# Kernel optimization log

Measured on AMD Instinct MI355X. Metric: run time of the kernel, lower is better.

The kernel has to match this reference:

```python
import jax, jax.numpy as jnp
import numpy as np

HEADS = 8


def setup_inputs() -> dict:
    key = jax.random.key(0)
    ks = jax.random.split(key, 6)
    dim = 256
    s = 0.02
    return {
        "x": jax.random.normal(ks[0], (8, dim, 32, 32), jnp.float32),
        "w_qkv": jax.random.normal(ks[1], (3 * dim, dim), jnp.float32) * s,
        "w_out": jax.random.normal(ks[2], (dim, dim), jnp.float32) * s,
        "b_out": jnp.zeros((dim,), jnp.float32),
        "w_g1": jax.random.normal(ks[3], (dim // 4, dim), jnp.float32) * s,
        "b_g1": jnp.zeros((dim // 4,), jnp.float32),
        "w_g2": jax.random.normal(ks[4], (1, dim // 4), jnp.float32) * s,
        "b_g2": jnp.zeros((1,), jnp.float32),
    }


def _conv1x1(t, w, bias=None):
    # 1x1 conv == channel matmul
    y = jnp.einsum('bchw,oc->bohw', t, w)
    if bias is not None:
        y = y + bias[None, :, None, None]
    return y


def _forward(x, w_qkv, w_out, b_out, w_g1, b_g1, w_g2, b_g2):
    b, c, h, w = x.shape
    heads = HEADS
    d = c // heads
    n = h * w
    m = min(h, w)
    scale = d ** (-0.5)

    qkv = _conv1x1(x, w_qkv)  # [b, 3c, h, w]

    def to_heads(t):  # 'b (h d) x y -> b h (x y) d'
        return t.reshape(b, heads, d, n).transpose(0, 1, 3, 2)

    q, k, v = (to_heads(t) for t in jnp.split(qkv, 3, axis=1))

    attn = jax.nn.softmax(jnp.einsum('bhid,bhjd->bhij', q, k) * scale, axis=-1)

    # diagonal branch (anti-diagonal scores are computed in the original but
    # never used in the output -> omitted as dead code)
    q2d = q.reshape(b, heads, h, w, d)
    k2d = k.reshape(b, heads, h, w, d)
    q_dm = jnp.diagonal(q2d, axis1=2, axis2=3)  # [b, heads, d, m]
    k_dm = jnp.diagonal(k2d, axis1=2, axis2=3)
    diag_main = jnp.einsum('bhnd,bhmd->bhnm', q_dm, k_dm) * scale  # [b, heads, d, d]
    diag_vec = jnp.diagonal(diag_main.mean(axis=1), axis1=-2, axis2=-1)  # [b, d]
    diag_vec = jnp.pad(diag_vec, ((0, 0), (0, n - m)))  # [b, n] (d == m)

    DIAG_WEIGHT = 0.3
    enhanced = attn + DIAG_WEIGHT * diag_vec[:, None, :, None]

    out = jnp.einsum('bhij,bhjd->bhid', enhanced, v)  # [b, heads, n, d]
    out = out.reshape(b, heads, h, w, d).transpose(0, 1, 4, 2, 3).reshape(b, c, h, w)

    # left/right asymmetry gate
    mid = w // 2
    left = x[:, :, :, :mid]
    right = x[:, :, :, mid:]
    asym = jnp.abs(left - right[:, :, :, ::-1])  # [b, c, h, w/2]
    # adaptive_avg_pool2d (h, w/2) -> (h, w) with even w == width repeat by 2
    pooled = jnp.repeat(asym, 2, axis=3)
    g = _conv1x1(pooled, w_g1, b_g1)
    g = jax.nn.gelu(g, approximate=False)
    g = jax.nn.sigmoid(_conv1x1(g, w_g2, b_g2))  # [b, 1, h, w]

    out = out * (1.0 + g)
    return _conv1x1(out, w_out, b_out)


def reference(x, w_qkv, w_out, b_out, w_g1, b_g1, w_g2, b_g2):
    return _forward(x, w_qkv, w_out, b_out, w_g1, b_g1, w_g2, b_g2)
```

## Files before the change

### kernel.cpp

```cpp
#include <hip/hip_runtime.h>
#include <hip/hip_bf16.h>
#include <math.h>

#define B 8
#define C 256
#define HEADS 8
#define D 32
#define NPIX 1024
#define OC 768
#define SCALE 0.17677669529663687f
#define LOG2E 1.4426950408889634f

typedef unsigned int uint;
typedef unsigned short u16;
typedef __attribute__((ext_vector_type(8))) short bf16x8;
typedef __attribute__((ext_vector_type(4))) short bf16x4;
typedef __attribute__((ext_vector_type(4))) float f32x4;

static __device__ inline u16 f2bf(float f) {
  uint u = __float_as_uint(f);
  return (u16)((u + 0x7fffu + ((u >> 16) & 1u)) >> 16);
}
static __device__ inline float bfval(u16 v) { return __uint_as_float((uint)v << 16); }
static __device__ inline float bf_lo(uint u) { return __uint_as_float(u << 16); }
static __device__ inline float bf_hi(uint u) { return __uint_as_float(u & 0xffff0000u); }

static __device__ inline uint pk2(float lo, float hi) {
  union { __hip_bfloat162 h; uint u; } cv;
  cv.h = __float22bfloat162_rn(float2{lo, hi});
  return cv.u;
}

__global__ __launch_bounds__(256) void k_prep(
    const float* __restrict__ x, const float* __restrict__ wqkv,
    const float* __restrict__ wout,
    u16* __restrict__ WQ, u16* __restrict__ WO, u16* __restrict__ XT) {
  const int bid = blockIdx.x, t = threadIdx.x;
  __shared__ u16 tile[64][65];
  if (bid < 256) {
    const float* src;
    u16* dst;
    int base;
    if (bid < 192) { src = wqkv; dst = WQ; base = bid * 1024; }
    else           { src = wout; dst = WO; base = (bid - 192) * 1024; }
    float4 v = *(const float4*)(src + base + t * 4);
    uint2 pk = make_uint2((uint)f2bf(v.x) | ((uint)f2bf(v.y) << 16),
                          (uint)f2bf(v.z) | ((uint)f2bf(v.w) << 16));
    *(uint2*)(dst + base + t * 4) = pk;
    return;
  }
  const int id = bid - 256;
  const int pt = id & 15, ct = (id >> 4) & 3, b = id >> 6;
  {
    const int px = t & 63, cq = t >> 6;
    const float* xb = x + ((size_t)(b * C + ct * 64)) * NPIX + pt * 64;
#pragma unroll
    for (int m = 0; m < 16; ++m) {
      const int c = cq * 16 + m;
      tile[c][px] = f2bf(xb[(size_t)c * NPIX + px]);
    }
  }
  __syncthreads();
  {
    const int cc = t & 63, pq = t >> 6;
    u16* dst = XT + ((size_t)(b * NPIX + pt * 64)) * C + ct * 64;
#pragma unroll
    for (int m = 0; m < 16; ++m) {
      const int pix = pq * 16 + m;
      dst[(size_t)pix * C + cc] = tile[cc][pix];
    }
  }
}

__global__ __launch_bounds__(256) void k_qkv_mfma(
    const u16* __restrict__ XT, const u16* __restrict__ WQ,
    u16* __restrict__ Q, u16* __restrict__ Kk, u16* __restrict__ VT) {
  const int ob = blockIdx.x, pb = blockIdx.y, b = blockIdx.z;
  const int wv = threadIdx.x >> 6, lane = threadIdx.x & 63;
  const int quad = lane >> 4, l15 = lane & 15;
  const int part = ob >> 2;
  const int odl = (ob & 3) * 64 + wv * 16;
  const int hh = odl >> 5, d0 = odl & 31;
  const int bh = b * HEADS + hh;
  const int pix0 = pb * 128;

  const u16* arow = WQ + (size_t)(ob * 64 + wv * 16 + l15) * C;
  bf16x8 af[8];
#pragma unroll
  for (int kc = 0; kc < 8; ++kc)
    af[kc] = *(const bf16x8*)(arow + kc * 32 + quad * 8);

  const u16* xb = XT + (size_t)(b * NPIX + pix0) * C;
  f32x4 acc[8];
#pragma unroll
  for (int nt = 0; nt < 8; ++nt) acc[nt] = (f32x4){0.f, 0.f, 0.f, 0.f};

  for (int kc = 0; kc < 8; ++kc) {
#pragma unroll
    for (int nt = 0; nt < 8; ++nt) {
      bf16x8 bfr = *(const bf16x8*)(xb + (size_t)(nt * 16 + l15) * C +
                                    kc * 32 + quad * 8);
      acc[nt] = __builtin_amdgcn_mfma_f32_16x16x32_bf16(af[kc], bfr, acc[nt], 0, 0, 0);
    }
  }

  if (part == 0) {
    const float qs = SCALE * LOG2E;
    u16* dst = Q + (size_t)bh * NPIX * D;
#pragma unroll
    for (int nt = 0; nt < 8; ++nt) {
      const int pix = pix0 + nt * 16 + l15;
      uint2 pk = make_uint2(
          (uint)f2bf(acc[nt][0] * qs) | ((uint)f2bf(acc[nt][1] * qs) << 16),
          (uint)f2bf(acc[nt][2] * qs) | ((uint)f2bf(acc[nt][3] * qs) << 16));
      *(uint2*)(dst + (size_t)pix * D + d0 + 4 * quad) = pk;
    }
  } else if (part == 1) {
    u16* kfb = Kk + (size_t)bh * NPIX * D;
    const int lane_k8 = (((d0 >> 3) + (quad >> 1)) * 16 + l15) * 8 + (quad & 1) * 4;
#pragma unroll
    for (int nt = 0; nt < 8; ++nt) {
      uint2 pk = make_uint2(
          (uint)f2bf(acc[nt][0]) | ((uint)f2bf(acc[nt][1]) << 16),
          (uint)f2bf(acc[nt][2]) | ((uint)f2bf(acc[nt][3]) << 16));
      *(uint2*)(kfb + (size_t)(pb * 8 + nt) * 512 + lane_k8) = pk;
    }
  } else {
    u16* vb = VT + (size_t)bh * NPIX * D;
#pragma unroll
    for (int nt = 0; nt < 8; ++nt) {
      const int pix = pix0 + nt * 16 + l15;
      const int jb16 = pix >> 4, qa = (pix >> 2) & 3, m = pix & 3;
#pragma unroll
      for (int r = 0; r < 4; ++r) {
        const int d = d0 + 4 * quad + r;
        const int nta = d >> 4, l15a = d & 15;
        vb[((size_t)(jb16 * 2 + nta) * 64 + qa * 16 + l15a) * 4 + m] =
            f2bf(acc[nt][r]);
      }
    }
  }
}

__global__ __launch_bounds__(256) void k_red(
    const u16* __restrict__ Q, const u16* __restrict__ KF,
    const u16* __restrict__ VT, float* __restrict__ diagv,
    float* __restrict__ colsum) {
  const int bid = blockIdx.x, tid = threadIdx.x;
  __shared__ float red[256];
  if (bid < 8) {
    const int b = bid;
    const int hh = tid >> 5, dd = tid & 31;
    const u16* qb = Q + (size_t)(b * HEADS + hh) * NPIX * D;
    const u16* kb = KF + (size_t)(b * HEADS + hh) * NPIX * D;
    float s = 0.f;
#pragma unroll 4
    for (int t = 0; t < 32; ++t) {
      const int j = t * 33;
      float qv = bfval(qb[(size_t)j * D + dd]);
      float kv = bfval(kb[(size_t)(j >> 4) * 512 +
                          ((dd >> 3) * 16 + (j & 15)) * 8 + (dd & 7)]);
      s += qv * kv;
    }
    red[tid] = s;
    __syncthreads();
    if (tid < 32) {
      float v = 0.f;
#pragma unroll
      for (int h8 = 0; h8 < 8; ++h8) v += red[h8 * 32 + tid];
      diagv[b * 32 + tid] = v * (0.125f / LOG2E);
    }
  } else {
    const int bh = bid - 8;
    const int d = tid >> 3, sl = tid & 7;
    const int nta = d >> 4, l15a = d & 15;
    const u16* vb = VT + (size_t)bh * NPIX * D;
    float s = 0.f;
    for (int jb = 0; jb < 8; ++jb) {
      const int jb16 = sl * 8 + jb;
#pragma unroll
      for (int qa = 0; qa < 4; ++qa) {
        const uint2 u = *(const uint2*)(
            vb + ((size_t)(jb16 * 2 + nta) * 64 + qa * 16 + l15a) * 4);
        s += bf_lo(u.x) + bf_hi(u.x) + bf_lo(u.y) + bf_hi(u.y);
      }
    }
    red[tid] = s;
    __syncthreads();
    if (tid < 32) {
      float v = 0.f;
#pragma unroll
      for (int g = 0; g < 8; ++g) v += red[tid * 8 + g];
      colsum[bh * D + tid] = v;
    }
  }
}

__global__ __launch_bounds__(256, 4) void k_attn(
    const u16* __restrict__ Q, const u16* __restrict__ KF,
    const u16* __restrict__ VF, const float* __restrict__ diagv,
    const float* __restrict__ colsum, u16* __restrict__ AOT) {
  const int qc = blockIdx.x;
  const int bh = blockIdx.y;
  const int b = bh >> 3, hh = bh & 7;
  const int wv = threadIdx.x >> 6, lane = threadIdx.x & 63;
  const int quad = lane >> 4, l15 = lane & 15;
  const int i0 = qc * 64 + wv * 16;

  __shared__ u16 sbuf[2][4096];

  const u16* Qb  = Q  + (size_t)bh * NPIX * D;
  const u16* KFb = KF + (size_t)bh * NPIX * D;
  const u16* VFb = VF + (size_t)bh * NPIX * D;

  bf16x8 qfrag = *(const bf16x8*)(Qb + (size_t)(i0 + l15) * D + quad * 8);

  f32x4 oacc[2];
  oacc[0] = (f32x4){0.f, 0.f, 0.f, 0.f};
  oacc[1] = (f32x4){0.f, 0.f, 0.f, 0.f};
  float lacc[4] = {};

  const u16* gsrc = (wv < 2 ? KFb : VFb) + (wv & 1) * 1024 + lane * 8;
  u16* ldst[2] = { &sbuf[0][wv * 1024 + lane * 8],
                   &sbuf[1][wv * 1024 + lane * 8] };

  {
    uint4 a = *(const uint4*)(gsrc);
    uint4 c = *(const uint4*)(gsrc + 512);
    *(uint4*)(ldst[0]) = a;
    *(uint4*)(ldst[0] + 512) = c;
  }
  __syncthreads();

  int cur = 0;
  for (int it = 0; it < 16; ++it) {
    if (it < 15) {
      uint4 a = *(const uint4*)(gsrc + (size_t)(it + 1) * 2048);
      uint4 c = *(const uint4*)(gsrc + (size_t)(it + 1) * 2048 + 512);
      u16* ld = ldst[cur ^ 1];
      *(uint4*)(ld) = a;
      *(uint4*)(ld + 512) = c;
    }
    const u16* sK = &sbuf[cur][0];
    const u16* sV = &sbuf[cur][2048];

    f32x4 st[4];
#pragma unroll
    for (int jt = 0; jt < 4; ++jt) {
      bf16x8 kfrag = *(const bf16x8*)(sK + jt * 512 + lane * 8);
      st[jt] = __builtin_amdgcn_mfma_f32_16x16x32_bf16(
          kfrag, qfrag, (f32x4){0.f, 0.f, 0.f, 0.f}, 0, 0, 0);
    }

#pragma unroll
    for (int jt = 0; jt < 4; ++jt)
#pragma unroll
      for (int r = 0; r < 4; ++r) {
        float pv = exp2f(fminf(st[jt][r], 80.f));
        lacc[r] += pv;
        st[jt][r] = pv;
      }

    __builtin_amdgcn_s_setprio(1);
#pragma unroll
    for (int jt = 0; jt < 4; ++jt) {
      union { uint u[2]; bf16x4 v; } pa;
      pa.u[0] = pk2(st[jt][0], st[jt][1]);
      pa.u[1] = pk2(st[jt][2], st[jt][3]);
#pragma unroll
      for (int nt = 0; nt < 2; ++nt) {
        bf16x4 vfr = *(const bf16x4*)(sV + (jt * 2 + nt) * 256 + lane * 4);
        oacc[nt] = __builtin_amdgcn_mfma_f32_16x16x16bf16_1k(
            pa.v, vfr, oacc[nt], 0, 0, 0);
      }
    }
    __builtin_amdgcn_s_setprio(0);

    __syncthreads();
    cur ^= 1;
  }

  float lt = (lacc[0] + lacc[1]) + (lacc[2] + lacc[3]);
  lt += __shfl_xor(lt, 16, 64);
  lt += __shfl_xor(lt, 32, 64);
  const float linv = 1.f / lt;
  float rinv[4];
#pragma unroll
  for (int r = 0; r < 4; ++r) rinv[r] = __shfl(linv, quad * 4 + r, 64);

  const bool do_diag = (i0 < 32);
#pragma unroll
  for (int nt = 0; nt < 2; ++nt) {
    const int dch = hh * 32 + nt * 16 + l15;
    float cs = do_diag ? colsum[bh * D + (nt * 16 + l15)] : 0.f;
#pragma unroll
    for (int r = 0; r < 4; ++r) {
      const int irow = i0 + quad * 4 + r;
      float o = oacc[nt][r] * rinv[r];
      if (do_diag) o += 0.3f * diagv[b * 32 + irow] * cs;
      AOT[((size_t)b * NPIX + irow) * C + dch] = f2bf(o);
    }
  }
}

__global__ __launch_bounds__(256) void k_gate(
    const float* __restrict__ x,
    const float* __restrict__ wg1, const float* __restrict__ bg1,
    const float* __restrict__ wg2, const float* __restrict__ bg2,
    float* __restrict__ gate) {
  const int h = blockIdx.x, b = blockIdx.y, tid = threadIdx.x;
  __shared__ float pl[16 * 257];
  __shared__ float gl[16 * 65];

  {
    const int c = tid;
    const float* row = x + ((size_t)(b * C + c) * NPIX + h * 32);
    float v[32];
#pragma unroll
    for (int m = 0; m < 32; ++m) v[m] = row[m];
#pragma unroll
    for (int k = 0; k < 16; ++k) pl[k * 257 + c] = fabsf(v[k] - v[31 - k]);
  }
  __syncthreads();

  const int o16 = tid >> 4, k = tid & 15;
#pragma unroll 1
  for (int p = 0; p < 4; ++p) {
    const int o = p * 16 + o16;
    const float* wr = wg1 + o * C;
    float a0 = 0.f, a1 = 0.f, a2 = 0.f, a3 = 0.f;
#pragma unroll 4
    for (int c = 0; c < C; c += 4) {
      a0 += wr[c]     * pl[k * 257 + c];
      a1 += wr[c + 1] * pl[k * 257 + c + 1];
      a2 += wr[c + 2] * pl[k * 257 + c + 2];
      a3 += wr[c + 3] * pl[k * 257 + c + 3];
    }
    float a = bg1[o] + ((a0 + a1) + (a2 + a3));
    gl[k * 65 + o] = 0.5f * a * (1.f + erff(a * 0.70710678118654752f));
  }
  __syncthreads();

  if (tid < 16) {
    float s = bg2[0];
    for (int o = 0; o < 64; ++o)
      s += wg2[o] * gl[tid * 65 + o];
    gate[(b * 32 + h) * 16 + tid] = 1.f / (1.f + expf(-s));
  }
}

__global__ __launch_bounds__(256) void k_out_mfma(
    const u16* __restrict__ AOT, const u16* __restrict__ WO,
    const float* __restrict__ bout, const float* __restrict__ gate,
    float* __restrict__ out) {
  const int ob = blockIdx.x, pb = blockIdx.y, b = blockIdx.z;
  const int wv = threadIdx.x >> 6, lane = threadIdx.x & 63;
  const int quad = lane >> 4, l15 = lane & 15;
  const int o0 = ob * 64 + wv * 16;
  const int pix0 = pb * 128;

  const u16* arow = WO + (size_t)(o0 + l15) * C;
  bf16x8 af[8];
#pragma unroll
  for (int kc = 0; kc < 8; ++kc)
    af[kc] = *(const bf16x8*)(arow + kc * 32 + quad * 8);

  const u16* ab = AOT + (size_t)(b * NPIX + pix0) * C;
  f32x4 acc[8];
#pragma unroll
  for (int nt = 0; nt < 8; ++nt) acc[nt] = (f32x4){0.f, 0.f, 0.f, 0.f};

  for (int kc = 0; kc < 8; ++kc) {
#pragma unroll
    for (int nt = 0; nt < 8; ++nt) {
      bf16x8 bfr = *(const bf16x8*)(ab + (size_t)(nt * 16 + l15) * C +
                                    kc * 32 + quad * 8);
      acc[nt] = __builtin_amdgcn_mfma_f32_16x16x32_bf16(af[kc], bfr, acc[nt], 0, 0, 0);
    }
  }

#pragma unroll
  for (int nt = 0; nt < 8; ++nt) {
    const int pix = pix0 + nt * 16 + l15;
    const float gf = 1.f + gate[(b * 32 + (pix >> 5)) * 16 + ((pix & 31) >> 1)];
#pragma unroll
    for (int r = 0; r < 4; ++r) {
      const int o = o0 + 4 * quad + r;
      out[((size_t)b * C + o) * NPIX + pix] = acc[nt][r] * gf + bout[o];
    }
  }
}

extern "C" void kernel_launch(void* const* d_in, const int* in_sizes, int n_in,
                              void* d_out, int out_size, void* d_ws, size_t ws_size,
                              hipStream_t stream) {
  const float* x    = (const float*)d_in[0];
  const float* wqkv = (const float*)d_in[1];
  const float* wout = (const float*)d_in[2];
  const float* bout = (const float*)d_in[3];
  const float* wg1  = (const float*)d_in[4];
  const float* bg1  = (const float*)d_in[5];
  const float* wg2  = (const float*)d_in[6];
  const float* bg2  = (const float*)d_in[7];
  float* out = (float*)d_out;

  const size_t SZ = (size_t)B * HEADS * NPIX * D;
  u16* XT = (u16*)d_ws;
  u16* WQ = XT + SZ;
  u16* WO = WQ + (size_t)OC * C;
  u16* Q  = WO + (size_t)C * C;
  u16* Kq = Q + SZ;
  u16* VT = Kq + SZ;
  float* DIAG = (float*)(VT + SZ);
  float* COL  = DIAG + 256;
  float* GATE = COL + 2048;
  u16* AOT = XT;

  hipLaunchKernelGGL(k_prep, dim3(768), dim3(256), 0, stream,
                     x, wqkv, wout, WQ, WO, XT);
  hipLaunchKernelGGL(k_qkv_mfma, dim3(12, 8, B), dim3(256), 0, stream,
                     XT, WQ, Q, Kq, VT);
  hipLaunchKernelGGL(k_red, dim3(72), dim3(256), 0, stream,
                     Q, Kq, VT, DIAG, COL);
  hipLaunchKernelGGL(k_attn, dim3(16, 64), dim3(256), 0, stream,
                     Q, Kq, VT, DIAG, COL, AOT);
  hipLaunchKernelGGL(k_gate, dim3(32, B), dim3(256), 0, stream,
                     x, wg1, bg1, wg2, bg2, GATE);
  hipLaunchKernelGGL(k_out_mfma, dim3(4, 8, B), dim3(256), 0, stream,
                     AOT, WO, bout, GATE, out);
}
```

Baseline: 169.0 us.

## Store XT in MFMA fragment layout and widen attention blocks to 512 threads

The prep kernel now writes the transposed activations straight into an MFMA-fragment-ordered layout, so each lane in the QKV GEMM does one contiguous 16-byte load per fragment instead of a strided gather. Separately, the attention kernel moves to 512-thread blocks covering 128 queries. Each staged K/V tile is then shared by twice as many query rows, which halves the global K/V traffic per query, and each thread issues one load per stage. Risks: larger blocks may lower occupancy or raise register pressure, and any other consumer of the XT layout must match.

```diff
diff --git a/kernel.cpp b/kernel.cpp
--- a/kernel.cpp
+++ b/kernel.cpp
@@ -63,17 +63,18 @@
   __syncthreads();
   {
     const int cc = t & 63, pq = t >> 6;
-    u16* dst = XT + ((size_t)(b * NPIX + pt * 64)) * C + ct * 64;
-#pragma unroll
-    for (int m = 0; m < 16; ++m) {
-      const int pix = pq * 16 + m;
-      dst[(size_t)pix * C + cc] = tile[cc][pix];
-    }
+    const int c = ct * 64 + cc;
+    const int kc = c >> 5, quad = (c >> 3) & 3, mm = c & 7;
+    u16* dst = XT + ((size_t)((b * 64 + pt * 4 + pq) * 8 + kc) * 512 +
+                     quad * 128 + mm);
+#pragma unroll
+    for (int m = 0; m < 16; ++m)
+      dst[m * 8] = tile[cc][pq * 16 + m];
   }
 }
 
 __global__ __launch_bounds__(256) void k_qkv_mfma(
-    const u16* __restrict__ XT, const u16* __restrict__ WQ,
+    const u16* __restrict__ XTF, const u16* __restrict__ WQ,
     u16* __restrict__ Q, u16* __restrict__ Kk, u16* __restrict__ VT) {
   const int ob = blockIdx.x, pb = blockIdx.y, b = blockIdx.z;
   const int wv = threadIdx.x >> 6, lane = threadIdx.x & 63;
@@ -90,7 +91,7 @@
   for (int kc = 0; kc < 8; ++kc)
     af[kc] = *(const bf16x8*)(arow + kc * 32 + quad * 8);
 
-  const u16* xb = XT + (size_t)(b * NPIX + pix0) * C;
+  const u16* xb = XTF + (size_t)(b * 64 + pb * 8) * 8 * 512 + lane * 8;
   f32x4 acc[8];
 #pragma unroll
   for (int nt = 0; nt < 8; ++nt) acc[nt] = (f32x4){0.f, 0.f, 0.f, 0.f};
@@ -98,8 +99,7 @@
   for (int kc = 0; kc < 8; ++kc) {
 #pragma unroll
     for (int nt = 0; nt < 8; ++nt) {
-      bf16x8 bfr = *(const bf16x8*)(xb + (size_t)(nt * 16 + l15) * C +
-                                    kc * 32 + quad * 8);
+      bf16x8 bfr = *(const bf16x8*)(xb + (size_t)(nt * 8 + kc) * 512);
       acc[nt] = __builtin_amdgcn_mfma_f32_16x16x32_bf16(af[kc], bfr, acc[nt], 0, 0, 0);
     }
   }
@@ -196,7 +196,7 @@
   }
 }
 
-__global__ __launch_bounds__(256, 4) void k_attn(
+__global__ __launch_bounds__(512, 4) void k_attn(
     const u16* __restrict__ Q, const u16* __restrict__ KF,
     const u16* __restrict__ VF, const float* __restrict__ diagv,
     const float* __restrict__ colsum, u16* __restrict__ AOT) {
@@ -205,7 +205,7 @@
   const int b = bh >> 3, hh = bh & 7;
   const int wv = threadIdx.x >> 6, lane = threadIdx.x & 63;
   const int quad = lane >> 4, l15 = lane & 15;
-  const int i0 = qc * 64 + wv * 16;
+  const int i0 = qc * 128 + wv * 16;
 
   __shared__ u16 sbuf[2][4096];
 
@@ -220,27 +220,17 @@
   oacc[1] = (f32x4){0.f, 0.f, 0.f, 0.f};
   float lacc[4] = {};
 
-  const u16* gsrc = (wv < 2 ? KFb : VFb) + (wv & 1) * 1024 + lane * 8;
-  u16* ldst[2] = { &sbuf[0][wv * 1024 + lane * 8],
-                   &sbuf[1][wv * 1024 + lane * 8] };
-
-  {
-    uint4 a = *(const uint4*)(gsrc);
-    uint4 c = *(const uint4*)(gsrc + 512);
-    *(uint4*)(ldst[0]) = a;
-    *(uint4*)(ldst[0] + 512) = c;
-  }
+  const int soff = (wv >= 4 ? 2048 : 0) + (wv & 3) * 512 + lane * 8;
+  const u16* gsrc = (wv < 4 ? KFb : VFb) + (wv & 3) * 512 + lane * 8;
+  u16* ldst[2] = { &sbuf[0][soff], &sbuf[1][soff] };
+
+  *(uint4*)(ldst[0]) = *(const uint4*)(gsrc);
   __syncthreads();
 
   int cur = 0;
   for (int it = 0; it < 16; ++it) {
-    if (it < 15) {
-      uint4 a = *(const uint4*)(gsrc + (size_t)(it + 1) * 2048);
-      uint4 c = *(const uint4*)(gsrc + (size_t)(it + 1) * 2048 + 512);
-      u16* ld = ldst[cur ^ 1];
-      *(uint4*)(ld) = a;
-      *(uint4*)(ld + 512) = c;
-    }
+    if (it < 15)
+      *(uint4*)(ldst[cur ^ 1]) = *(const uint4*)(gsrc + (size_t)(it + 1) * 2048);
     const u16* sK = &sbuf[cur][0];
     const u16* sV = &sbuf[cur][2048];
 
@@ -422,7 +412,7 @@
                      XT, WQ, Q, Kq, VT);
   hipLaunchKernelGGL(k_red, dim3(72), dim3(256), 0, stream,
                      Q, Kq, VT, DIAG, COL);
-  hipLaunchKernelGGL(k_attn, dim3(16, 64), dim3(256), 0, stream,
+  hipLaunchKernelGGL(k_attn, dim3(8, 64), dim3(512), 0, stream,
                      Q, Kq, VT, DIAG, COL, AOT);
   hipLaunchKernelGGL(k_gate, dim3(32, B), dim3(256), 0, stream,
                      x, wg1, bg1, wg2, bg2, GATE);
```

After: 156.4 us. -7.5%, faster.
